# Kernel tuning notes

Hardware: AMD Instinct MI355X
Metric: run time of the kernel (lower is better)

The kernel has to match this reference:

```python
import jax, jax.numpy as jnp
import numpy as np

KERNEL_MUL = 2.0
KERNEL_NUM = 5
EPS = 1e-5


def _gaussian_kernel(a, b):
    # a: [n, d], b: [m, d]. Squared L2 distances via dot-product trick
    # (same math as the tiled (n,m,d) subtraction in the original, without
    # materializing the rank-3 intermediate).
    sq_a = jnp.sum(a * a, axis=1)  # [n]
    sq_b = jnp.sum(b * b, axis=1)  # [m]
    d2 = sq_a[:, None] + sq_b[None, :] - 2.0 * (a @ b.T)  # [n, m]
    d2 = jnp.maximum(d2, 0.0)
    n_samples = a.shape[0] + b.shape[0]
    # bandwidth from detached distances (L2_distance.data in torch)
    bw = jax.lax.stop_gradient(jnp.sum(d2)) / (n_samples ** 2 - n_samples)
    bw = bw / (KERNEL_MUL ** (KERNEL_NUM // 2))
    bws = bw * (KERNEL_MUL ** jnp.arange(KERNEL_NUM, dtype=d2.dtype)) + EPS  # [K]
    # sum of K Gaussian kernels, fused over the bandwidth axis
    k = jnp.sum(jnp.exp(-d2[None, :, :] / bws[:, None, None]), axis=0)  # [n, m]
    return k


def setup_inputs() -> dict:
    key = jax.random.key(0)
    kx, ky = jax.random.split(key)
    x = jax.random.normal(kx, (4096, 256), dtype=jnp.float32)
    y = jax.random.normal(ky, (4096, 256), dtype=jnp.float32)
    return {"x": x, "y": y}


def reference(x, y):
    xx = _gaussian_kernel(x, x).mean()
    yy = _gaussian_kernel(y, y).mean()
    xy = _gaussian_kernel(x, y).mean()
    mmd = xx + yy - 2.0 * xy
    return mmd
```

## Files before the change

kernel.cpp:

```cpp
#include <hip/hip_runtime.h>

#define N 4096
#define D 256
#define BT 128
#define NB2 32
#define TRI 528
#define TOTAL 2080
#define BK 32
#define KT (D / BK)

typedef __attribute__((ext_vector_type(8))) _Float16 f16x8;
typedef __attribute__((ext_vector_type(4))) _Float16 f16x4;
typedef __attribute__((ext_vector_type(4))) float f32x4;

__device__ __forceinline__ void gld_lds16(const void* g, void* l) {
    __builtin_amdgcn_global_load_lds(
        (const __attribute__((address_space(1))) unsigned int*)g,
        (__attribute__((address_space(3))) unsigned int*)l, 16, 0, 0);
}

__global__ void k_cvt(const float* __restrict__ x, const float* __restrict__ y,
                      _Float16* __restrict__ xc, _Float16* __restrict__ yc,
                      float* __restrict__ sq, float* __restrict__ pb) {
    const int mat = blockIdx.y;
    const float* src = mat ? y : x;
    _Float16* dst = mat ? yc : xc;
    const int w = threadIdx.x >> 6, lane = threadIdx.x & 63;
    const int r0 = blockIdx.x * 32 + w * 8;
    __shared__ float lds[4][256];
    float4 colacc = {0.f, 0.f, 0.f, 0.f};
    #pragma unroll
    for (int r = 0; r < 8; ++r) {
        const int row = r0 + r;
        const float4 v = *(const float4*)(src + (size_t)row * D + lane * 4);
        f16x4 h;
        h.x = (_Float16)v.x; h.y = (_Float16)v.y;
        h.z = (_Float16)v.z; h.w = (_Float16)v.w;
        *(f16x4*)(dst + (size_t)row * D + lane * 4) = h;
        float s = v.x * v.x + v.y * v.y + v.z * v.z + v.w * v.w;
        #pragma unroll
        for (int off = 32; off; off >>= 1) s += __shfl_down(s, off);
        if (lane == 0) sq[mat * N + row] = s;
        colacc.x += v.x; colacc.y += v.y; colacc.z += v.z; colacc.w += v.w;
    }
    *(float4*)&lds[w][lane * 4] = colacc;
    __syncthreads();
    const int t = threadIdx.x;
    pb[(mat * (N / 32) + blockIdx.x) * 256 + t] =
        lds[0][t] + lds[1][t] + lds[2][t] + lds[3][t];
}

__global__ void k_prep(const float* __restrict__ sq, const float* __restrict__ pb,
                       float* __restrict__ coef, double* __restrict__ acc) {
    const int t = threadIdx.x;
    double sx = 0, sy = 0;
    for (int i = t; i < N; i += 256) { sx += (double)sq[i]; sy += (double)sq[N + i]; }
    double cx = 0, cy = 0;
    for (int b = 0; b < N / 32; ++b) {
        cx += (double)pb[b * 256 + t];
        cy += (double)pb[(N / 32 + b) * 256 + t];
    }
    double v[5] = {sx, sy, cx * cx, cy * cy, cx * cy};
    #pragma unroll
    for (int k = 0; k < 5; ++k)
        for (int off = 32; off; off >>= 1) v[k] += __shfl_down(v[k], off);
    __shared__ double red[4][5];
    const int w = t >> 6, lane = t & 63;
    if (lane == 0) for (int k = 0; k < 5; ++k) red[w][k] = v[k];
    __syncthreads();
    if (t == 0) {
        double Sx = 0, Sy = 0, Cxx = 0, Cyy = 0, Cxy = 0;
        for (int q = 0; q < 4; ++q) {
            Sx += red[q][0]; Sy += red[q][1];
            Cxx += red[q][2]; Cyy += red[q][3]; Cxy += red[q][4];
        }
        const double ns = 2.0 * N;
        const double denom = ns * ns - ns;
        const double sd[3] = {
            2.0 * N * Sx - 2.0 * Cxx,
            2.0 * N * Sy - 2.0 * Cyy,
            (double)N * Sx + (double)N * Sy - 2.0 * Cxy };
        const double L2E = 1.4426950408889634;
        for (int q = 0; q < 3; ++q) {
            const double bw = sd[q] / denom / 4.0;
            coef[q] = (float)(L2E / (16.0 * bw + 1e-5));
        }
        acc[0] = 0.0; acc[1] = 0.0; acc[2] = 0.0;
    }
}

__global__ __launch_bounds__(256) void k_mmd(
    const _Float16* __restrict__ xc, const _Float16* __restrict__ yc,
    const float* __restrict__ sq, const float* __restrict__ coefs,
    double* __restrict__ acc) {
    __shared__ __align__(16) _Float16 As[2 * BT * BK];
    __shared__ __align__(16) _Float16 Bs[2 * BT * BK];
    __shared__ double red[4];

    const int bid = (blockIdx.x & 7) * (TOTAL / 8) + (blockIdx.x >> 3);

    int p, b;
    if (bid < TRI)          { p = 0; b = bid; }
    else if (bid < 2 * TRI) { p = 1; b = bid - TRI; }
    else                    { p = 2; b = bid - 2 * TRI; }
    const _Float16* A = (p == 1) ? yc : xc;
    const _Float16* B = (p == 0) ? xc : yc;
    const float* sqA = (p == 1) ? sq + N : sq;
    const float* sqB = (p == 0) ? sq : sq + N;
    const float c4 = coefs[p];

    int bi, bj;
    if (p < 2) {
        int rem = b, r = 0;
        while (rem >= NB2 - r) { rem -= NB2 - r; ++r; }
        bi = r; bj = r + rem;
    } else { bi = b >> 5; bj = b & 31; }

    const int tid = threadIdx.x;
    const int lane = tid & 63, w = tid >> 6;

    const int srow = tid >> 2;
    const int sc = (tid & 3) ^ (srow & 3) ^ ((srow >> 2) & 3);
    const char* gA = (const char*)A + (size_t)(bi * BT + srow) * (D * 2) + sc * 16;
    const char* gB = (const char*)B + (size_t)(bj * BT + srow) * (D * 2) + sc * 16;
    char* lA = (char*)As + tid * 16;
    char* lB = (char*)Bs + tid * 16;

#define STAGE(kt, buf) do { \
        const int kb_ = (kt) * (BK * 2); const int co_ = (buf) * 8192; \
        gld_lds16(gA + kb_, lA + co_); \
        gld_lds16(gA + kb_ + 64 * (D * 2), lA + co_ + 4096); \
        gld_lds16(gB + kb_, lB + co_); \
        gld_lds16(gB + kb_ + 64 * (D * 2), lB + co_ + 4096); \
    } while (0)

    const int wr = (w >> 1) * 64, wc = (w & 1) * 64;
    const int fr = lane & 15;
    const int lg = lane >> 4;
    const int ch = (lg ^ (fr & 3) ^ (fr >> 2)) * 16;
    const char* rA = (const char*)As + (wr + fr) * 64 + ch;
    const char* rB = (const char*)Bs + (wc + fr) * 64 + ch;

    f32x4 accv[4][4];
    #pragma unroll
    for (int m = 0; m < 4; ++m)
        #pragma unroll
        for (int n = 0; n < 4; ++n) accv[m][n] = {0.f, 0.f, 0.f, 0.f};

    STAGE(0, 0);
    asm volatile("s_waitcnt vmcnt(0)" ::: "memory");
    __builtin_amdgcn_s_barrier();
    __builtin_amdgcn_sched_barrier(0);

    #pragma unroll
    for (int kt = 0; kt < KT; ++kt) {
        if (kt + 1 < KT) STAGE(kt + 1, (kt + 1) & 1);
        const int co = (kt & 1) * 8192;
        f16x8 af[4], bf[4];
        #pragma unroll
        for (int m = 0; m < 4; ++m)
            af[m] = *(const f16x8*)(rA + co + m * 1024);
        #pragma unroll
        for (int n = 0; n < 4; ++n)
            bf[n] = *(const f16x8*)(rB + co + n * 1024);
        asm volatile("s_waitcnt lgkmcnt(0)" ::: "memory");
        __builtin_amdgcn_sched_barrier(0);
        #pragma unroll
        for (int m = 0; m < 4; ++m)
            #pragma unroll
            for (int n = 0; n < 4; ++n)
                accv[m][n] = __builtin_amdgcn_mfma_f32_16x16x32_f16(
                    af[m], bf[n], accv[m][n], 0, 0, 0);
        if (kt + 1 < KT) {
            asm volatile("s_waitcnt vmcnt(0)" ::: "memory");
            __builtin_amdgcn_s_barrier();
            __builtin_amdgcn_sched_barrier(0);
        }
    }

    const float c2x = 2.f * c4;
    const int row0 = bi * BT + wr + lg * 4;
    const int col0 = bj * BT + wc + fr;
    float asa[4][4], bsb[4];
    #pragma unroll
    for (int m = 0; m < 4; ++m) {
        const f32x4 sa = *(const f32x4*)(sqA + row0 + m * 16);
        #pragma unroll
        for (int i = 0; i < 4; ++i) asa[m][i] = sa[i] * c4;
    }
    #pragma unroll
    for (int n = 0; n < 4; ++n) bsb[n] = sqB[col0 + n * 16] * c4;
    float s = 0.f;
    #pragma unroll
    for (int m = 0; m < 4; ++m)
        #pragma unroll
        for (int n = 0; n < 4; ++n)
            #pragma unroll
            for (int i = 0; i < 4; ++i) {
                float arg = fmaf(accv[m][n][i], c2x, -(asa[m][i] + bsb[n]));
                arg = fminf(arg, 0.f);
                const float u = __builtin_amdgcn_exp2f(arg);
                const float u2 = u * u, u4 = u2 * u2;
                const float u8 = u4 * u4, u16 = u8 * u8;
                s += (u + u2) + (u4 + u8) + u16;
            }
    if (p < 2 && bi != bj) s *= 2.f;

    double sd = (double)s;
    #pragma unroll
    for (int off = 32; off; off >>= 1) sd += __shfl_down(sd, off);
    if (lane == 0) red[w] = sd;
    __syncthreads();
    if (tid == 0) atomicAdd(&acc[p], red[0] + red[1] + red[2] + red[3]);
#undef STAGE
}

__global__ void k_final(const double* __restrict__ acc, float* __restrict__ out) {
    const double inv = 1.0 / ((double)N * (double)N);
    out[0] = (float)((acc[0] + acc[1] - 2.0 * acc[2]) * inv);
}

extern "C" void kernel_launch(void* const* d_in, const int* in_sizes, int n_in,
                              void* d_out, int out_size, void* d_ws, size_t ws_size,
                              hipStream_t stream) {
    const float* x = (const float*)d_in[0];
    const float* y = (const float*)d_in[1];
    float* out = (float*)d_out;

    char* base = (char*)d_ws;
    double* acc = (double*)base;
    float*  sq  = (float*)(base + 64);
    float*  coef = (float*)(base + 64 + 32768);
    float*  pb  = (float*)(base + 65536);
    _Float16* xc = (_Float16*)(base + 65536 + 262144);
    _Float16* yc = (_Float16*)(base + 65536 + 262144 + N * D * 2);

    k_cvt<<<dim3(N / 32, 2), 256, 0, stream>>>(x, y, xc, yc, sq, pb);
    k_prep<<<1, 256, 0, stream>>>(sq, pb, coef, acc);
    k_mmd<<<TOTAL, 256, 0, stream>>>(xc, yc, sq, coef, acc);
    k_final<<<1, 1, 0, stream>>>(acc, out);
}
```

Before: 119.7 us.

## Load MFMA fragments directly from global memory and fold final reduction into GEMM kernel

Removes the LDS double-buffered staging (global_load_lds, barriers, swizzle) in the MMD GEMM kernel. Each wave now reads its f16 A/B fragments straight from global memory, relying on L1/L2 for reuse across waves. Separately, the final-combine kernel is replaced by a last-block-done counter with atomics, saving one launch. The trade-off is more global/L2 traffic and less latency hiding in exchange for no LDS use or barriers, which may raise occupancy.

Measured after the change: 176.6 us. 1.48x slower.

```diff
diff --git a/kernel.cpp b/kernel.cpp
--- a/kernel.cpp
+++ b/kernel.cpp
@@ -6,18 +6,10 @@
 #define NB2 32
 #define TRI 528
 #define TOTAL 2080
-#define BK 32
-#define KT (D / BK)
 
 typedef __attribute__((ext_vector_type(8))) _Float16 f16x8;
 typedef __attribute__((ext_vector_type(4))) _Float16 f16x4;
 typedef __attribute__((ext_vector_type(4))) float f32x4;
-
-__device__ __forceinline__ void gld_lds16(const void* g, void* l) {
-    __builtin_amdgcn_global_load_lds(
-        (const __attribute__((address_space(1))) unsigned int*)g,
-        (__attribute__((address_space(3))) unsigned int*)l, 16, 0, 0);
-}
 
 __global__ void k_cvt(const float* __restrict__ x, const float* __restrict__ y,
                       _Float16* __restrict__ xc, _Float16* __restrict__ yc,
@@ -51,7 +43,8 @@
 }
 
 __global__ void k_prep(const float* __restrict__ sq, const float* __restrict__ pb,
-                       float* __restrict__ coef, double* __restrict__ acc) {
+                       float* __restrict__ coef, double* __restrict__ acc,
+                       int* __restrict__ cnt) {
     const int t = threadIdx.x;
     double sx = 0, sy = 0;
     for (int i = t; i < N; i += 256) { sx += (double)sq[i]; sy += (double)sq[N + i]; }
@@ -86,15 +79,14 @@
             coef[q] = (float)(L2E / (16.0 * bw + 1e-5));
         }
         acc[0] = 0.0; acc[1] = 0.0; acc[2] = 0.0;
+        *cnt = 0;
     }
 }
 
 __global__ __launch_bounds__(256) void k_mmd(
     const _Float16* __restrict__ xc, const _Float16* __restrict__ yc,
     const float* __restrict__ sq, const float* __restrict__ coefs,
-    double* __restrict__ acc) {
-    __shared__ __align__(16) _Float16 As[2 * BT * BK];
-    __shared__ __align__(16) _Float16 Bs[2 * BT * BK];
+    double* __restrict__ acc, int* __restrict__ cnt, float* __restrict__ out) {
     __shared__ double red[4];
 
     const int bid = (blockIdx.x & 7) * (TOTAL / 8) + (blockIdx.x >> 3);
@@ -118,28 +110,12 @@
 
     const int tid = threadIdx.x;
     const int lane = tid & 63, w = tid >> 6;
-
-    const int srow = tid >> 2;
-    const int sc = (tid & 3) ^ (srow & 3) ^ ((srow >> 2) & 3);
-    const char* gA = (const char*)A + (size_t)(bi * BT + srow) * (D * 2) + sc * 16;
-    const char* gB = (const char*)B + (size_t)(bj * BT + srow) * (D * 2) + sc * 16;
-    char* lA = (char*)As + tid * 16;
-    char* lB = (char*)Bs + tid * 16;
-
-#define STAGE(kt, buf) do { \
-        const int kb_ = (kt) * (BK * 2); const int co_ = (buf) * 8192; \
-        gld_lds16(gA + kb_, lA + co_); \
-        gld_lds16(gA + kb_ + 64 * (D * 2), lA + co_ + 4096); \
-        gld_lds16(gB + kb_, lB + co_); \
-        gld_lds16(gB + kb_ + 64 * (D * 2), lB + co_ + 4096); \
-    } while (0)
-
     const int wr = (w >> 1) * 64, wc = (w & 1) * 64;
     const int fr = lane & 15;
     const int lg = lane >> 4;
-    const int ch = (lg ^ (fr & 3) ^ (fr >> 2)) * 16;
-    const char* rA = (const char*)As + (wr + fr) * 64 + ch;
-    const char* rB = (const char*)Bs + (wc + fr) * 64 + ch;
+
+    const char* pA = (const char*)A + (size_t)(bi * BT + wr + fr) * (D * 2) + lg * 16;
+    const char* pB = (const char*)B + (size_t)(bj * BT + wc + fr) * (D * 2) + lg * 16;
 
     f32x4 accv[4][4];
     #pragma unroll
@@ -147,63 +123,43 @@
         #pragma unroll
         for (int n = 0; n < 4; ++n) accv[m][n] = {0.f, 0.f, 0.f, 0.f};
 
-    STAGE(0, 0);
-    asm volatile("s_waitcnt vmcnt(0)" ::: "memory");
-    __builtin_amdgcn_s_barrier();
-    __builtin_amdgcn_sched_barrier(0);
-
-    #pragma unroll
-    for (int kt = 0; kt < KT; ++kt) {
-        if (kt + 1 < KT) STAGE(kt + 1, (kt + 1) & 1);
-        const int co = (kt & 1) * 8192;
+    #pragma unroll
+    for (int kk = 0; kk < 8; ++kk) {
         f16x8 af[4], bf[4];
         #pragma unroll
         for (int m = 0; m < 4; ++m)
-            af[m] = *(const f16x8*)(rA + co + m * 1024);
+            af[m] = *(const f16x8*)(pA + m * (16 * D * 2) + kk * 64);
         #pragma unroll
         for (int n = 0; n < 4; ++n)
-            bf[n] = *(const f16x8*)(rB + co + n * 1024);
-        asm volatile("s_waitcnt lgkmcnt(0)" ::: "memory");
-        __builtin_amdgcn_sched_barrier(0);
+            bf[n] = *(const f16x8*)(pB + n * (16 * D * 2) + kk * 64);
         #pragma unroll
         for (int m = 0; m < 4; ++m)
             #pragma unroll
             for (int n = 0; n < 4; ++n)
                 accv[m][n] = __builtin_amdgcn_mfma_f32_16x16x32_f16(
                     af[m], bf[n], accv[m][n], 0, 0, 0);
-        if (kt + 1 < KT) {
-            asm volatile("s_waitcnt vmcnt(0)" ::: "memory");
-            __builtin_amdgcn_s_barrier();
-            __builtin_amdgcn_sched_barrier(0);
-        }
-    }
-
-    const float c2x = 2.f * c4;
+    }
+
     const int row0 = bi * BT + wr + lg * 4;
     const int col0 = bj * BT + wc + fr;
-    float asa[4][4], bsb[4];
+    float s = 0.f;
     #pragma unroll
     for (int m = 0; m < 4; ++m) {
         const f32x4 sa = *(const f32x4*)(sqA + row0 + m * 16);
         #pragma unroll
-        for (int i = 0; i < 4; ++i) asa[m][i] = sa[i] * c4;
-    }
-    #pragma unroll
-    for (int n = 0; n < 4; ++n) bsb[n] = sqB[col0 + n * 16] * c4;
-    float s = 0.f;
-    #pragma unroll
-    for (int m = 0; m < 4; ++m)
-        #pragma unroll
-        for (int n = 0; n < 4; ++n)
+        for (int n = 0; n < 4; ++n) {
+            const float sb = sqB[col0 + n * 16];
             #pragma unroll
             for (int i = 0; i < 4; ++i) {
-                float arg = fmaf(accv[m][n][i], c2x, -(asa[m][i] + bsb[n]));
-                arg = fminf(arg, 0.f);
+                const float arg =
+                    fminf((2.f * accv[m][n][i] - sa[i] - sb) * c4, 0.f);
                 const float u = __builtin_amdgcn_exp2f(arg);
                 const float u2 = u * u, u4 = u2 * u2;
                 const float u8 = u4 * u4, u16 = u8 * u8;
                 s += (u + u2) + (u4 + u8) + u16;
             }
+        }
+    }
     if (p < 2 && bi != bj) s *= 2.f;
 
     double sd = (double)s;
@@ -211,13 +167,17 @@
     for (int off = 32; off; off >>= 1) sd += __shfl_down(sd, off);
     if (lane == 0) red[w] = sd;
     __syncthreads();
-    if (tid == 0) atomicAdd(&acc[p], red[0] + red[1] + red[2] + red[3]);
-#undef STAGE
-}
-
-__global__ void k_final(const double* __restrict__ acc, float* __restrict__ out) {
-    const double inv = 1.0 / ((double)N * (double)N);
-    out[0] = (float)((acc[0] + acc[1] - 2.0 * acc[2]) * inv);
+    if (tid == 0) {
+        atomicAdd(&acc[p], red[0] + red[1] + red[2] + red[3]);
+        __threadfence();
+        if (atomicAdd(cnt, 1) == TOTAL - 1) {
+            __threadfence();
+            const double a0 = atomicAdd(&acc[0], 0.0);
+            const double a1 = atomicAdd(&acc[1], 0.0);
+            const double a2 = atomicAdd(&acc[2], 0.0);
+            out[0] = (float)((a0 + a1 - 2.0 * a2) / ((double)N * (double)N));
+        }
+    }
 }
 
 extern "C" void kernel_launch(void* const* d_in, const int* in_sizes, int n_in,
@@ -229,14 +189,14 @@
 
     char* base = (char*)d_ws;
     double* acc = (double*)base;
-    float*  sq  = (float*)(base + 64);
-    float*  coef = (float*)(base + 64 + 32768);
-    float*  pb  = (float*)(base + 65536);
-    _Float16* xc = (_Float16*)(base + 65536 + 262144);
-    _Float16* yc = (_Float16*)(base + 65536 + 262144 + N * D * 2);
+    float*  coef = (float*)(base + 32);
+    int*    cnt  = (int*)(base + 48);
+    float*  sq   = (float*)(base + 64);
+    float*  pb   = (float*)(base + 64 + 32768);
+    _Float16* xc = (_Float16*)(base + 294976);
+    _Float16* yc = (_Float16*)(base + 294976 + (size_t)N * D * 2);
 
     k_cvt<<<dim3(N / 32, 2), 256, 0, stream>>>(x, y, xc, yc, sq, pb);
-    k_prep<<<1, 256, 0, stream>>>(sq, pb, coef, acc);
-    k_mmd<<<TOTAL, 256, 0, stream>>>(xc, yc, sq, coef, acc);
-    k_final<<<1, 1, 0, stream>>>(acc, out);
-}
+    k_prep<<<1, 256, 0, stream>>>(sq, pb, coef, acc, cnt);
+    k_mmd<<<TOTAL, 256, 0, stream>>>(xc, yc, sq, coef, acc, cnt, out);
+}
```
